# Performance work log

Measured on AMD Instinct MI355X. Metric: run time of the kernel, lower is better.

The kernel has to match this reference:

```python
import jax, jax.numpy as jnp
import numpy as np
import itertools

R = 32  # voxel resolution
B, CIN, COUT, N, SD = 4, 32, 64, 32768, 256


def group_norm(x, gamma, beta, eps=1e-5):
    # torch GroupNorm with g = min(8, C) adjusted for divisibility
    C = x.shape[1]
    g = min(8, C)
    while g > 1 and C % g:
        g -= 1
    b = x.shape[0]
    xs = x.reshape(b, g, C // g, -1)
    mu = xs.mean(axis=(2, 3), keepdims=True)
    var = xs.var(axis=(2, 3), keepdims=True)
    xn = ((xs - mu) / jnp.sqrt(var + eps)).reshape(x.shape)
    shp = (1, C) + (1,) * (x.ndim - 2)
    return xn * gamma.reshape(shp) + beta.reshape(shp)


def conv1x1(w, x):  # w: (O, C), x: (B, C, N)
    return jnp.einsum('oc,bcn->bon', w, x)


def conv3d(x, w):  # x: (B,C,D,H,W), w: (O,I,3,3,3), padding 1
    return jax.lax.conv_general_dilated(x, w, (1, 1, 1), 'SAME',
                                        dimension_numbers=('NCDHW', 'OIDHW', 'NCDHW'))


def normalize_coords(coords):  # (B,N,3) -> [0, R-1]
    vmin = coords.min(axis=1, keepdims=True)
    vmax = coords.max(axis=1, keepdims=True)
    return (coords - vmin) / jnp.maximum(vmax - vmin, 1e-8) * (R - 1)


def voxelize(feats_bcn, norm):  # average voxelization via scatter-add
    b, C, n = feats_bcn.shape
    idx = jnp.clip(jnp.round(norm), 0, R - 1).astype(jnp.int32)  # (B,N,3)
    flat = (idx[..., 0] * R + idx[..., 1]) * R + idx[..., 2]  # (B,N)
    f_bnc = feats_bcn.transpose(0, 2, 1)
    seg = jax.vmap(lambda f, i: jax.ops.segment_sum(f, i, num_segments=R ** 3))(f_bnc, flat)
    cnt = jax.vmap(lambda i: jax.ops.segment_sum(jnp.ones((n,), feats_bcn.dtype), i, num_segments=R ** 3))(flat)
    vox = seg / jnp.maximum(cnt, 1.0)[..., None]  # (B, R^3, C)
    return vox.transpose(0, 2, 1).reshape(b, C, R, R, R)


def devoxelize(vox, norm):  # trilinear interpolation gather
    b, C = vox.shape[:2]
    n = norm.shape[1]
    f = jnp.clip(norm, 0.0, R - 1)
    x0 = jnp.floor(f)
    fr = f - x0
    x0i = x0.astype(jnp.int32)
    idxs, wts = [], []
    for d in itertools.product((0, 1), repeat=3):
        dv = jnp.array(d, jnp.int32)
        ci = jnp.minimum(x0i + dv, R - 1)  # (B,N,3)
        w = jnp.prod(jnp.where(jnp.array(d, bool), fr, 1.0 - fr), axis=-1)  # (B,N)
        idxs.append((ci[..., 0] * R + ci[..., 1]) * R + ci[..., 2])
        wts.append(w)
    idx8 = jnp.stack(idxs, axis=-1)  # (B,N,8)
    w8 = jnp.stack(wts, axis=-1)  # (B,N,8)
    vf = vox.reshape(b, C, R ** 3)
    g = jnp.take_along_axis(vf, idx8.reshape(b, 1, n * 8), axis=2).reshape(b, C, n, 8)
    return jnp.einsum('bcnk,bnk->bcn', g, w8)


def setup_inputs() -> dict:
    key = jax.random.key(0)
    ks = jax.random.split(key, 12)
    s = 0.05
    return {
        'feats': jax.random.normal(ks[0], (B, CIN, N), jnp.float32),
        'coords': jax.random.uniform(ks[1], (B, N, 3), jnp.float32),
        'style': jax.random.normal(ks[2], (B, SD), jnp.float32),
        'w_pin': jax.random.normal(ks[3], (COUT, CIN), jnp.float32) * s,
        'g_pin': jnp.ones((COUT,), jnp.float32), 'b_pin': jnp.zeros((COUT,), jnp.float32),
        'w_v1': jax.random.normal(ks[4], (COUT, COUT, 3, 3, 3), jnp.float32) * s,
        'g_v1': jnp.ones((COUT,), jnp.float32), 'b_v1': jnp.zeros((COUT,), jnp.float32),
        'w_v2': jax.random.normal(ks[5], (COUT, COUT, 3, 3, 3), jnp.float32) * s,
        'g_v2': jnp.ones((COUT,), jnp.float32), 'b_v2': jnp.zeros((COUT,), jnp.float32),
        'w_fuse': jax.random.normal(ks[6], (COUT, COUT), jnp.float32) * s,
        'g_f': jnp.ones((COUT,), jnp.float32), 'b_f': jnp.zeros((COUT,), jnp.float32),
        'w_skip': jax.random.normal(ks[7], (COUT, CIN), jnp.float32) * s,
        'w_as': jax.random.normal(ks[8], (COUT, SD), jnp.float32) * s,
        'b_as': jnp.zeros((COUT,), jnp.float32),
        'w_ab': jax.random.normal(ks[9], (COUT, SD), jnp.float32) * s,
        'b_ab': jnp.zeros((COUT,), jnp.float32),
    }


def reference(feats, coords, style, w_pin, g_pin, b_pin, w_v1, g_v1, b_v1,
              w_v2, g_v2, b_v2, w_fuse, g_f, b_f, w_skip, w_as, b_as, w_ab, b_ab):
    silu = jax.nn.silu
    x_in = silu(group_norm(conv1x1(w_pin, feats), g_pin, b_pin))  # point_in
    norm = normalize_coords(coords)
    vox = voxelize(x_in, norm)
    vox = silu(group_norm(conv3d(vox, w_v1), g_v1, b_v1))
    vox = silu(group_norm(conv3d(vox, w_v2), g_v2, b_v2))
    devox = devoxelize(vox, norm)
    out = silu(group_norm(conv1x1(w_fuse, devox), g_f, b_f))  # fuse
    out = out + conv1x1(w_skip, feats)  # skip (c_in != c_out)
    s = (style @ w_as.T + b_as)[..., None]  # AdaIN scale (B, C, 1)
    bb = (style @ w_ab.T + b_ab)[..., None]
    return out * (1.0 + s) + bb
```

## Files before the change

kernel.cpp:

```cpp
#include <hip/hip_runtime.h>
#include <hip/hip_bf16.h>
#include <math.h>

#define RR   32
#define RB   4
#define CIN  32
#define CO   64
#define NP   32768
#define SD   256
#define NVOX (RR*RR*RR)
#define GRP  8
#define CPG  8
#define GN_CNT 262144.0f
#define PR   34
#define PSLICE (PR*PR*CO)
#define PROW   (PR*CO)
#define PVOL   ((size_t)PR*PR*PR*CO)

typedef __attribute__((ext_vector_type(8))) short short8;
typedef __attribute__((ext_vector_type(4))) float f32x4;
typedef __attribute__((ext_vector_type(16))) float f32x16;

__device__ inline float silu_f(float x){ return x / (1.f + __expf(-x)); }
__device__ inline float bf2f(ushort u){ uint v = ((uint)u)<<16; return *(float*)&v; }
__device__ inline ushort f2bf(float x){ __hip_bfloat16 h = __float2bfloat16(x); return *(ushort*)&h; }

__device__ inline void wpack_dev(const float* __restrict__ w, short* __restrict__ wp, int i){
    int l  = i & 63;
    int nt = (i>>6) & 1;
    int kc = (i>>7) & 3;
    int t  = i>>9;
    int oc = nt*32 + (l&31);
    int cib = kc*16 + (l>>5)*8;
    ushort out[8];
    #pragma unroll
    for (int j=0;j<8;j++) out[j] = f2bf(w[((oc*CO + cib + j))*27 + t]);
    *(uint4*)(wp + (size_t)i*8) = *(uint4*)out;
}

__global__ __launch_bounds__(256) void k_prep(const float* __restrict__ w_v1, const float* __restrict__ w_v2,
                      short* __restrict__ wp1, short* __restrict__ wp2,
                      const float* __restrict__ style, const float* __restrict__ w_as,
                      const float* __restrict__ b_as, const float* __restrict__ w_ab,
                      const float* __restrict__ b_ab, float* __restrict__ ada_s,
                      float* __restrict__ ada_b, float* __restrict__ stats,
                      const float* __restrict__ coords, float* __restrict__ vmm){
    __shared__ float smn[256][3], smx[256][3];
    int blk = blockIdx.x, t = threadIdx.x;
    if (blk < 54){
        int i = blk*256 + t;
        if (i < 27*4*2*64) wpack_dev(w_v1, wp1, i);
    } else if (blk < 108){
        int i = (blk-54)*256 + t;
        if (i < 27*4*2*64) wpack_dev(w_v2, wp2, i);
    } else if (blk == 108){
        stats[t] = 0.f;
        int b = t >> 6, o = t & 63;
        const float* st = style + b*SD;
        float accs = b_as[o], accb = b_ab[o];
        for (int k=0;k<SD;k++){ float sv = st[k]; accs += sv*w_as[o*SD+k]; accb += sv*w_ab[o*SD+k]; }
        ada_s[t]=accs; ada_b[t]=accb;
    } else {
        int b = blk - 109;
        float mn[3]={1e30f,1e30f,1e30f}, mx[3]={-1e30f,-1e30f,-1e30f};
        const float* cp = coords + (size_t)b*NP*3;
        for (int n=t;n<NP;n+=256){
            #pragma unroll
            for(int d=0;d<3;d++){ float v = cp[n*3+d]; mn[d]=fminf(mn[d],v); mx[d]=fmaxf(mx[d],v);}
        }
        #pragma unroll
        for(int d=0;d<3;d++){ smn[t][d]=mn[d]; smx[t][d]=mx[d]; }
        __syncthreads();
        for(int s=128;s>0;s>>=1){
            if(t<s){
                #pragma unroll
                for(int d=0;d<3;d++){
                    smn[t][d]=fminf(smn[t][d],smn[t+s][d]);
                    smx[t][d]=fmaxf(smx[t][d],smx[t+s][d]);
                }
            }
            __syncthreads();
        }
        if(t<3){ vmm[b*6+t]=smn[0][t]; vmm[b*6+3+t]=smx[0][t]; }
    }
}

__global__ __launch_bounds__(256) void k_count(const float* __restrict__ coords, const float* __restrict__ vmm,
                        int* __restrict__ pid, int* __restrict__ cnt){
    int p = blockIdx.x*256 + threadIdx.x;
    int b = p >> 15, n = p & (NP-1);
    const float* cp = coords + (size_t)(b*NP + n)*3;
    int id[3];
    #pragma unroll
    for(int d=0;d<3;d++){
        float vmin = vmm[b*6+d], vmax = vmm[b*6+3+d];
        float nr = (cp[d]-vmin)/fmaxf(vmax-vmin,1e-8f)*(RR-1);
        int ii = (int)rintf(nr);
        id[d] = min(max(ii,0),RR-1);
    }
    int flat = (id[0]*RR + id[1])*RR + id[2];
    pid[p] = flat;
    atomicAdd(&cnt[(b<<15)+flat], 1);
}

__global__ __launch_bounds__(1024) void k_scan(const int* __restrict__ cnt, int* __restrict__ offs,
                        int* __restrict__ cursor){
    int b = blockIdx.x, t = threadIdx.x;
    const int* c = cnt + (b<<15);
    int base = t*32;
    int pref[32];
    int s = 0;
    #pragma unroll
    for (int k4=0;k4<8;k4++){
        int4 q = *(const int4*)(c + base + k4*4);
        pref[k4*4+0]=s; s+=q.x;
        pref[k4*4+1]=s; s+=q.y;
        pref[k4*4+2]=s; s+=q.z;
        pref[k4*4+3]=s; s+=q.w;
    }
    int lane = t & 63, w = t >> 6;
    int inc = s;
    #pragma unroll
    for (int off=1; off<64; off<<=1){ int u = __shfl_up(inc, off); if (lane>=off) inc += u; }
    __shared__ int wsum[16];
    if (lane==63) wsum[w]=inc;
    __syncthreads();
    int wexcl=0;
    for (int i=0;i<w;i++) wexcl += wsum[i];
    int texcl = wexcl + inc - s;
    int* o = offs + (b<<15) + base;
    int* cu = cursor + (b<<15) + base;
    #pragma unroll
    for (int k=0;k<32;k++){ int v = texcl + pref[k]; o[k]=v; cu[k]=v; }
}

__global__ __launch_bounds__(256) void k_fill(const int* __restrict__ pid, int* __restrict__ cursor,
                       int* __restrict__ slotmap){
    int p = blockIdx.x*256 + threadIdx.x;
    int b = p >> 15;
    int v = pid[p];
    int slot = atomicAdd(&cursor[(b<<15)+v], 1);
    slotmap[p] = slot;
}

__global__ __launch_bounds__(256) void k_pin(const float* __restrict__ feats, const float* __restrict__ w_pin,
                      const int* __restrict__ slotmap,
                      ushort* __restrict__ ybuf, float* __restrict__ stats){
    __shared__ float sred[GRP*2];
    int t = threadIdx.x;
    if (t<GRP*2) sred[t]=0.f;
    __syncthreads();
    int l = t & 63, wv = t >> 6;
    int lc = l & 31, h = l >> 5;
    int p = blockIdx.x*128 + wv*32 + lc;
    int b = p >> 15, n = p & (NP-1);
    short8 aw[2][2];
    #pragma unroll
    for (int nt=0;nt<2;nt++)
    #pragma unroll
    for (int kc=0;kc<2;kc++){
        ushort tmp[8];
        #pragma unroll
        for (int j=0;j<8;j++) tmp[j]=f2bf(w_pin[(nt*32+lc)*CIN + kc*16 + h*8 + j]);
        aw[nt][kc]=*(short8*)tmp;
    }
    const float* fp = feats + (size_t)b*CIN*NP + n;
    short8 bf[2];
    #pragma unroll
    for (int kc=0;kc<2;kc++){
        ushort tmp[8];
        #pragma unroll
        for (int j=0;j<8;j++) tmp[j]=f2bf(fp[(size_t)(kc*16+h*8+j)*NP]);
        bf[kc]=*(short8*)tmp;
    }
    f32x16 acc0={}, acc1={};
    #pragma unroll
    for (int kc=0;kc<2;kc++){
        acc0 = __builtin_amdgcn_mfma_f32_32x32x16_bf16(aw[0][kc], bf[kc], acc0, 0,0,0);
        acc1 = __builtin_amdgcn_mfma_f32_32x32x16_bf16(aw[1][kc], bf[kc], acc1, 0,0,0);
    }
    int slot = slotmap[p];
    ushort* yo = ybuf + ((size_t)(b<<15) + slot)*CO;
    float sg[8], qg[8];
    #pragma unroll
    for (int nt=0;nt<2;nt++){
        #pragma unroll
        for (int q=0;q<4;q++){
            ushort pk[4]; float s=0.f, qq=0.f;
            #pragma unroll
            for (int j=0;j<4;j++){
                float v = nt ? acc1[q*4+j] : acc0[q*4+j];
                pk[j]=f2bf(v); s+=v; qq+=v*v;
            }
            *(uint2*)(yo + nt*32 + q*8 + h*4) = *(uint2*)pk;
            sg[nt*4+q]=s; qg[nt*4+q]=qq;
        }
    }
    #pragma unroll
    for (int g=0;g<8;g++){
        float s=sg[g], q=qg[g];
        #pragma unroll
        for (int off=1; off<64; off<<=1){ s+=__shfl_xor(s,off); q+=__shfl_xor(q,off); }
        if (l==0){ atomicAdd(&sred[g*2],s); atomicAdd(&sred[g*2+1],q); }
    }
    __syncthreads();
    if (t<GRP){ atomicAdd(&stats[(b*GRP+t)*2], sred[t*2]); atomicAdd(&stats[(b*GRP+t)*2+1], sred[t*2+1]); }
}

__global__ __launch_bounds__(256) void k_gather_pad(const ushort* __restrict__ ybuf, const int* __restrict__ offs,
                             const float* __restrict__ stats,
                             const float* __restrict__ gamma, const float* __restrict__ beta,
                             ushort* __restrict__ P){
    int i = blockIdx.x*256 + threadIdx.x;
    int c8 = i & 7;
    int vox = (i>>3) & (NVOX-1);
    int b = i >> 18;
    float s = stats[(b*GRP+c8)*2], qq = stats[(b*GRP+c8)*2+1];
    float m = s/GN_CNT;
    float inv = rsqrtf(qq/GN_CNT - m*m + 1e-5f);
    float ga[8], be[8];
    #pragma unroll
    for (int k=0;k<8;k++){ ga[k]=gamma[c8*8+k]*inv; be[k]=beta[c8*8+k]-m*ga[k]; }
    int o0 = offs[(b<<15)+vox];
    int o1 = (vox==NVOX-1) ? NP : offs[(b<<15)+vox+1];
    float acc[8];
    #pragma unroll
    for (int k=0;k<8;k++) acc[k]=0.f;
    for (int j=o0; j<o1; j++){
        uint4 raw = *(const uint4*)(ybuf + ((size_t)((b<<15)+j))*CO + c8*8);
        ushort* us = (ushort*)&raw;
        #pragma unroll
        for (int k=0;k<8;k++){
            float x = bf2f(us[k])*ga[k] + be[k];
            acc[k] += silu_f(x);
        }
    }
    float rc = (o1>o0) ? 1.f/(float)(o1-o0) : 0.f;
    ushort out[8];
    #pragma unroll
    for (int k=0;k<8;k++) out[k]=f2bf(acc[k]*rc);
    int u = vox>>10, v = (vox>>5)&31, w = vox&31;
    size_t pd = ((size_t)b*PVOL) + (size_t)(u+1)*PSLICE + (v+1)*PROW + (w+1)*CO + c8*8;
    *(uint4*)(P + pd) = *(uint4*)out;
}

__global__ __launch_bounds__(256, 2) void k_conv_mfma(const __hip_bfloat16* __restrict__ P,
                        const short* __restrict__ wpack,
                        __hip_bfloat16* __restrict__ outv, float* __restrict__ stats){
    __shared__ __align__(16) char lds[10*4352 + 24576];
    char* wlds = lds + 10*4352;
    int t = threadIdx.x;
    int blk = blockIdx.x;
    int vt = blk & 3;
    int u  = (blk >> 2) & 31;
    int b  = blk >> 7;
    int v0 = vt*8;

    const ushort* Pp = (const ushort*)P;
    int l  = t & 63;
    int wv = t >> 6;
    int lr = l & 31;
    int lh = l >> 5;

    f32x16 acc00 = {}, acc01 = {}, acc10 = {}, acc11 = {};

    for (int dz = 0; dz < 3; dz++){
        for (int i = t; i < 2720; i += 256){
            int r = i / 272;
            int chunk = i - r*272;
            size_t src = (size_t)b*PVOL + (size_t)(u+dz)*PSLICE + (size_t)(v0+r)*PROW + (size_t)chunk*8;
            uint4 val = *(const uint4*)(Pp + src);
            int vx = chunk >> 3;
            int colb = (chunk & 7) << 4;
            *(uint4*)(lds + r*4352 + vx*128 + (colb ^ ((vx&7)<<4))) = val;
        }
        for (int dy = 0; dy < 3; dy++){
            const uint4* wsrc = (const uint4*)(wpack + (size_t)(dz*9 + dy*3)*4096);
            uint4* wdst = (uint4*)wlds;
            #pragma unroll
            for (int i=0;i<6;i++) wdst[t + i*256] = wsrc[t + i*256];
            __syncthreads();
            #pragma unroll
            for (int dx = 0; dx < 3; dx++){
                int vx = lr + dx;
                int sw = (vx & 7) << 4;
                int ra = (2*wv + dy)*4352 + vx*128;
                int wb = dx*8192 + l*16;
                #pragma unroll
                for (int kc = 0; kc < 4; kc++){
                    short8 bw0 = *(const short8*)(wlds + wb + kc*2048);
                    short8 bw1 = *(const short8*)(wlds + wb + kc*2048 + 1024);
                    int col = (kc*32 + lh*16) ^ sw;
                    short8 av0 = *(const short8*)(lds + ra + col);
                    short8 av1 = *(const short8*)(lds + ra + 4352 + col);
                    acc00 = __builtin_amdgcn_mfma_f32_32x32x16_bf16(av0, bw0, acc00, 0, 0, 0);
                    acc01 = __builtin_amdgcn_mfma_f32_32x32x16_bf16(av0, bw1, acc01, 0, 0, 0);
                    acc10 = __builtin_amdgcn_mfma_f32_32x32x16_bf16(av1, bw0, acc10, 0, 0, 0);
                    acc11 = __builtin_amdgcn_mfma_f32_32x32x16_bf16(av1, bw1, acc11, 0, 0, 0);
                }
            }
            __syncthreads();
        }
    }

    ushort* ob = (ushort*)outv;
    float s0 = 0.f, q0 = 0.f, s1 = 0.f, q1 = 0.f;
    size_t vrow0 = ((size_t)(b*32 + u)*32 + v0 + 2*wv);
    #pragma unroll
    for (int reg = 0; reg < 16; reg++){
        int x = (reg&3) + 8*(reg>>2) + 4*lh;
        float a, c;
        a = acc00[reg]; c = acc01[reg];
        s0 += a; q0 += a*a; s1 += c; q1 += c*c;
        ob[(vrow0*32 + x)*CO + lr]      = f2bf(a);
        ob[(vrow0*32 + x)*CO + 32 + lr] = f2bf(c);
        a = acc10[reg]; c = acc11[reg];
        s0 += a; q0 += a*a; s1 += c; q1 += c*c;
        ob[((vrow0+1)*32 + x)*CO + lr]      = f2bf(a);
        ob[((vrow0+1)*32 + x)*CO + 32 + lr] = f2bf(c);
    }
    #pragma unroll
    for (int off : {1,2,4,32}){
        s0 += __shfl_xor(s0, off); q0 += __shfl_xor(q0, off);
        s1 += __shfl_xor(s1, off); q1 += __shfl_xor(q1, off);
    }
    if (lh==0 && (lr&7)==0){
        int g0 = lr>>3;
        atomicAdd(&stats[(b*GRP+g0)*2],     s0);
        atomicAdd(&stats[(b*GRP+g0)*2+1],   q0);
        atomicAdd(&stats[(b*GRP+4+g0)*2],   s1);
        atomicAdd(&stats[(b*GRP+4+g0)*2+1], q1);
    }
}

__global__ __launch_bounds__(256) void k_gnfin_cast(const __hip_bfloat16* __restrict__ raw, const float* __restrict__ stats,
                        const float* __restrict__ gamma, const float* __restrict__ beta,
                        __hip_bfloat16* __restrict__ P){
    int i = blockIdx.x*256 + threadIdx.x;
    int c8 = i & 7;
    int vox = (i>>3) & (NVOX-1);
    int b = i >> 18;
    float s = stats[(b*GRP+c8)*2], qq = stats[(b*GRP+c8)*2+1];
    float m = s/GN_CNT;
    float inv = rsqrtf(qq/GN_CNT - m*m + 1e-5f);
    uint4 rv = *(const uint4*)((const ushort*)raw + ((size_t)i)*8);
    ushort* us = (ushort*)&rv;
    ushort out[8];
    #pragma unroll
    for (int j=0;j<8;j++){
        int c = c8*8+j;
        float x = (bf2f(us[j]) - m)*inv*gamma[c] + beta[c];
        out[j] = f2bf(silu_f(x));
    }
    int u = vox>>10, v = (vox>>5)&31, w = vox&31;
    size_t pd = ((size_t)b*PVOL) + (size_t)(u+1)*PSLICE + (v+1)*PROW + (w+1)*CO + c8*8;
    *(uint4*)((ushort*)P + pd) = *(uint4*)out;
}

__global__ __launch_bounds__(256) void k_devox_fuse(const __hip_bfloat16* __restrict__ vox_, const float* __restrict__ coords,
                             const float* __restrict__ vmm, const float* __restrict__ wf,
                             const float* __restrict__ st2, const float* __restrict__ g_v2,
                             const float* __restrict__ b_v2,
                             ushort* __restrict__ obuf, float* __restrict__ stats){
    __shared__ float sred[GRP*2];
    int t = threadIdx.x;
    if (t<GRP*2) sred[t]=0.f;
    __syncthreads();
    int l = t & 63, wv = t >> 6;
    int lc = l & 31, h = l >> 5;
    int p = blockIdx.x*128 + wv*32 + lc;
    int b = p >> 15, n = p & (NP-1);
    short8 aw[2][4];
    #pragma unroll
    for (int nt=0;nt<2;nt++)
    #pragma unroll
    for (int kc=0;kc<4;kc++){
        ushort tmp[8];
        #pragma unroll
        for (int j=0;j<8;j++) tmp[j]=f2bf(wf[(nt*32+lc)*CO + kc*16 + h*8 + j]);
        aw[nt][kc]=*(short8*)tmp;
    }
    float ga[4][8], be[4][8];
    #pragma unroll
    for (int kc=0;kc<4;kc++){
        int g = kc*2 + h;
        float s = st2[(b*GRP+g)*2], qq = st2[(b*GRP+g)*2+1];
        float m = s/GN_CNT;
        float inv = rsqrtf(qq/GN_CNT - m*m + 1e-5f);
        #pragma unroll
        for (int j=0;j<8;j++){
            int c = kc*16 + h*8 + j;
            ga[kc][j] = g_v2[c]*inv;
            be[kc][j] = b_v2[c] - m*ga[kc][j];
        }
    }
    const float* cp = coords + (size_t)(b*NP+n)*3;
    float fr[3]; int x0[3];
    #pragma unroll
    for(int d=0;d<3;d++){
        float vmin=vmm[b*6+d], vmax=vmm[b*6+3+d];
        float nr = (cp[d]-vmin)/fmaxf(vmax-vmin,1e-8f)*(RR-1);
        nr = fminf(fmaxf(nr,0.f),(float)(RR-1));
        float fl = floorf(nr);
        x0[d]=(int)fl; fr[d]=nr-fl;
    }
    float dev[4][8] = {};
    const ushort* vb = (const ushort*)vox_ + (size_t)b*NVOX*CO;
    #pragma unroll
    for (int k=0;k<8;k++){
        int d0=(k>>2)&1, d1=(k>>1)&1, d2=k&1;
        int i0=min(x0[0]+d0,RR-1), i1=min(x0[1]+d1,RR-1), i2=min(x0[2]+d2,RR-1);
        float w = (d0?fr[0]:1.f-fr[0])*(d1?fr[1]:1.f-fr[1])*(d2?fr[2]:1.f-fr[2]);
        const ushort* vp = vb + (size_t)((i0*RR+i1)*RR+i2)*CO + h*8;
        #pragma unroll
        for (int kc=0;kc<4;kc++){
            uint4 rv = *(const uint4*)(vp + kc*16);
            ushort* us = (ushort*)&rv;
            #pragma unroll
            for (int j=0;j<8;j++){
                float x = bf2f(us[j])*ga[kc][j] + be[kc][j];
                dev[kc][j] += w * silu_f(x);
            }
        }
    }
    short8 bf[4];
    #pragma unroll
    for (int kc=0;kc<4;kc++){
        ushort tmp[8];
        #pragma unroll
        for (int j=0;j<8;j++) tmp[j]=f2bf(dev[kc][j]);
        bf[kc]=*(short8*)tmp;
    }
    f32x16 acc0={}, acc1={};
    #pragma unroll
    for (int kc=0;kc<4;kc++){
        acc0 = __builtin_amdgcn_mfma_f32_32x32x16_bf16(aw[0][kc], bf[kc], acc0, 0,0,0);
        acc1 = __builtin_amdgcn_mfma_f32_32x32x16_bf16(aw[1][kc], bf[kc], acc1, 0,0,0);
    }
    ushort* op = obuf + (size_t)p*CO;
    float sg[8], qg[8];
    #pragma unroll
    for (int nt=0;nt<2;nt++){
        #pragma unroll
        for (int q=0;q<4;q++){
            ushort pk[4]; float s=0.f, qq=0.f;
            #pragma unroll
            for (int j=0;j<4;j++){
                float v = nt ? acc1[q*4+j] : acc0[q*4+j];
                pk[j]=f2bf(v); s+=v; qq+=v*v;
            }
            *(uint2*)(op + nt*32 + q*8 + h*4) = *(uint2*)pk;
            sg[nt*4+q]=s; qg[nt*4+q]=qq;
        }
    }
    #pragma unroll
    for (int g=0;g<8;g++){
        float s=sg[g], q=qg[g];
        #pragma unroll
        for (int off=1; off<64; off<<=1){ s+=__shfl_xor(s,off); q+=__shfl_xor(q,off); }
        if (l==0){ atomicAdd(&sred[g*2],s); atomicAdd(&sred[g*2+1],q); }
    }
    __syncthreads();
    if (t<GRP){ atomicAdd(&stats[(b*GRP+t)*2], sred[t*2]); atomicAdd(&stats[(b*GRP+t)*2+1], sred[t*2+1]); }
}

__global__ __launch_bounds__(256) void k_final(const ushort* __restrict__ obuf, const float* __restrict__ stats,
                        const float* __restrict__ gamma, const float* __restrict__ beta,
                        const float* __restrict__ feats, const float* __restrict__ wskip,
                        const float* __restrict__ ada_s, const float* __restrict__ ada_b,
                        float* __restrict__ out){
    int t = threadIdx.x;
    int l = t & 63, wv = t >> 6;
    int lc = l & 31, h = l >> 5;
    int p = blockIdx.x*128 + wv*32 + lc;
    int b = p >> 15, n = p & (NP-1);
    short8 aw[2][2];
    #pragma unroll
    for (int nt=0;nt<2;nt++)
    #pragma unroll
    for (int kc=0;kc<2;kc++){
        ushort tmp[8];
        #pragma unroll
        for (int j=0;j<8;j++) tmp[j]=f2bf(wskip[(nt*32+lc)*CIN + kc*16 + h*8 + j]);
        aw[nt][kc]=*(short8*)tmp;
    }
    const float* fp = feats + (size_t)b*CIN*NP + n;
    short8 bf[2];
    #pragma unroll
    for (int kc=0;kc<2;kc++){
        ushort tmp[8];
        #pragma unroll
        for (int j=0;j<8;j++) tmp[j]=f2bf(fp[(size_t)(kc*16+h*8+j)*NP]);
        bf[kc]=*(short8*)tmp;
    }
    f32x16 acc0={}, acc1={};
    #pragma unroll
    for (int kc=0;kc<2;kc++){
        acc0 = __builtin_amdgcn_mfma_f32_32x32x16_bf16(aw[0][kc], bf[kc], acc0, 0,0,0);
        acc1 = __builtin_amdgcn_mfma_f32_32x32x16_bf16(aw[1][kc], bf[kc], acc1, 0,0,0);
    }
    float mean[GRP], inv[GRP];
    #pragma unroll
    for (int g=0; g<GRP; g++){
        float s=stats[(b*GRP+g)*2], q=stats[(b*GRP+g)*2+1];
        float m=s/GN_CNT;
        mean[g]=m; inv[g]=rsqrtf(q/GN_CNT - m*m + 1e-5f);
    }
    const ushort* ip = obuf + (size_t)p*CO;
    float* op = out + (size_t)b*CO*NP + n;
    #pragma unroll
    for (int nt=0;nt<2;nt++){
        #pragma unroll
        for (int q=0;q<4;q++){
            uint2 raw = *(const uint2*)(ip + nt*32 + q*8 + h*4);
            ushort* us = (ushort*)&raw;
            int g = nt*4 + q;
            #pragma unroll
            for (int j=0;j<4;j++){
                int oc = nt*32 + q*8 + h*4 + j;
                float u = (bf2f(us[j]) - mean[g])*inv[g]*gamma[oc] + beta[oc];
                u = silu_f(u);
                float sk = nt ? acc1[q*4+j] : acc0[q*4+j];
                float s = ada_s[b*CO+oc], bb = ada_b[b*CO+oc];
                op[(size_t)oc*NP] = (u+sk)*(1.f+s)+bb;
            }
        }
    }
}

extern "C" void kernel_launch(void* const* d_in, const int* in_sizes, int n_in,
                              void* d_out, int out_size, void* d_ws, size_t ws_size,
                              hipStream_t stream){
    const float* feats =(const float*)d_in[0];
    const float* coords=(const float*)d_in[1];
    const float* style =(const float*)d_in[2];
    const float* w_pin =(const float*)d_in[3];
    const float* g_pin =(const float*)d_in[4];
    const float* b_pin =(const float*)d_in[5];
    const float* w_v1  =(const float*)d_in[6];
    const float* g_v1  =(const float*)d_in[7];
    const float* b_v1  =(const float*)d_in[8];
    const float* w_v2  =(const float*)d_in[9];
    const float* g_v2  =(const float*)d_in[10];
    const float* b_v2  =(const float*)d_in[11];
    const float* w_fuse=(const float*)d_in[12];
    const float* g_f   =(const float*)d_in[13];
    const float* b_f   =(const float*)d_in[14];
    const float* w_skip=(const float*)d_in[15];
    const float* w_as  =(const float*)d_in[16];
    const float* b_as  =(const float*)d_in[17];
    const float* w_ab  =(const float*)d_in[18];
    const float* b_ab  =(const float*)d_in[19];
    float* out=(float*)d_out;
    char* ws =(char*)d_ws;

    ushort* ybuf  = (ushort*)ws;
    ushort* Pvol  = (ushort*)(ws + 16777216);
    ushort* raw   = (ushort*)(ws + 16777216 + 20123648);
    char*   small = ws + 16777216 + 20123648 + 16777216;
    float* stats  = (float*)small;
    float* vmm    = stats + 256;
    float* ada_s  = vmm + 24;
    float* ada_b  = ada_s + RB*CO;
    short* wp1    = (short*)(ada_b + RB*CO);
    short* wp2    = wp1 + 27*4*2*64*8;
    int*   pid    = (int*)(wp2 + 27*4*2*64*8);
    int*   cnt    = pid + RB*NP;
    int*   offs   = cnt + RB*NVOX;
    int*   cursor = offs + RB*NVOX;
    int*   slotmap= cursor + RB*NVOX;
    ushort* obuf  = ybuf;

    float* st0 = stats;
    float* st1 = stats + 64;
    float* st2 = stats + 128;
    float* st3 = stats + 192;

    hipMemsetAsync(cnt, 0, (size_t)RB*NVOX*sizeof(int), stream);
    hipMemsetAsync(Pvol, 0, (size_t)RB*PVOL*sizeof(ushort), stream);

    k_prep<<<113,256,0,stream>>>(w_v1,w_v2,wp1,wp2,style,w_as,b_as,w_ab,b_ab,
                                 ada_s,ada_b,stats,coords,vmm);
    k_count<<<RB*NP/256,256,0,stream>>>(coords,vmm,pid,cnt);
    k_scan<<<RB,1024,0,stream>>>(cnt,offs,cursor);
    k_fill<<<RB*NP/256,256,0,stream>>>(pid,cursor,slotmap);
    k_pin<<<RB*NP/128,256,0,stream>>>(feats,w_pin,slotmap,ybuf,st0);
    k_gather_pad<<<RB*NVOX*8/256,256,0,stream>>>(ybuf,offs,st0,g_pin,b_pin,Pvol);

    k_conv_mfma<<<RB*RR*4,256,0,stream>>>((const __hip_bfloat16*)Pvol, wp1, (__hip_bfloat16*)raw, st1);
    k_gnfin_cast<<<RB*NVOX*8/256,256,0,stream>>>((const __hip_bfloat16*)raw, st1, g_v1, b_v1, (__hip_bfloat16*)Pvol);
    k_conv_mfma<<<RB*RR*4,256,0,stream>>>((const __hip_bfloat16*)Pvol, wp2, (__hip_bfloat16*)raw, st2);

    k_devox_fuse<<<RB*NP/128,256,0,stream>>>((const __hip_bfloat16*)raw, coords, vmm, w_fuse,
                                             st2, g_v2, b_v2, obuf, st3);
    k_final<<<RB*NP/128,256,0,stream>>>(obuf, st3, g_f, b_f, feats, w_skip, ada_s, ada_b, out);
}
```

Before: 385.5 us.

## Process devoxelization in voxel-sorted point order for gather locality

Normalized coordinates are computed once in k_count and scattered into voxel-sorted order in k_fill. k_devox_fuse then walks points in sorted order, so neighbouring threads read nearby voxels in the trilinear gather. k_final maps each point back through slotmap to read the fused output. This adds an extra scattered float4 write pass and an indirect read in the final kernel, and the workspace must be large enough for the two new float4 buffers.

```diff
diff --git a/kernel.cpp b/kernel.cpp
--- a/kernel.cpp
+++ b/kernel.cpp
@@ -86,20 +86,23 @@
 }
 
 __global__ __launch_bounds__(256) void k_count(const float* __restrict__ coords, const float* __restrict__ vmm,
-                        int* __restrict__ pid, int* __restrict__ cnt){
+                        int* __restrict__ pid, int* __restrict__ cnt, float4* __restrict__ nrm){
     int p = blockIdx.x*256 + threadIdx.x;
     int b = p >> 15, n = p & (NP-1);
     const float* cp = coords + (size_t)(b*NP + n)*3;
     int id[3];
+    float nc[3];
     #pragma unroll
     for(int d=0;d<3;d++){
         float vmin = vmm[b*6+d], vmax = vmm[b*6+3+d];
         float nr = (cp[d]-vmin)/fmaxf(vmax-vmin,1e-8f)*(RR-1);
+        nc[d] = fminf(fmaxf(nr,0.f),(float)(RR-1));
         int ii = (int)rintf(nr);
         id[d] = min(max(ii,0),RR-1);
     }
     int flat = (id[0]*RR + id[1])*RR + id[2];
     pid[p] = flat;
+    nrm[p] = make_float4(nc[0],nc[1],nc[2],0.f);
     atomicAdd(&cnt[(b<<15)+flat], 1);
 }
 
@@ -135,12 +138,14 @@
 }
 
 __global__ __launch_bounds__(256) void k_fill(const int* __restrict__ pid, int* __restrict__ cursor,
-                       int* __restrict__ slotmap){
+                       int* __restrict__ slotmap, const float4* __restrict__ nrm,
+                       float4* __restrict__ nrm_s){
     int p = blockIdx.x*256 + threadIdx.x;
     int b = p >> 15;
     int v = pid[p];
     int slot = atomicAdd(&cursor[(b<<15)+v], 1);
     slotmap[p] = slot;
+    nrm_s[(b<<15)+slot] = nrm[p];
 }
 
 __global__ __launch_bounds__(256) void k_pin(const float* __restrict__ feats, const float* __restrict__ w_pin,
@@ -357,8 +362,8 @@
     *(uint4*)((ushort*)P + pd) = *(uint4*)out;
 }
 
-__global__ __launch_bounds__(256) void k_devox_fuse(const __hip_bfloat16* __restrict__ vox_, const float* __restrict__ coords,
-                             const float* __restrict__ vmm, const float* __restrict__ wf,
+__global__ __launch_bounds__(256) void k_devox_fuse(const __hip_bfloat16* __restrict__ vox_,
+                             const float4* __restrict__ nrm_s, const float* __restrict__ wf,
                              const float* __restrict__ st2, const float* __restrict__ g_v2,
                              const float* __restrict__ b_v2,
                              ushort* __restrict__ obuf, float* __restrict__ stats){
@@ -368,8 +373,8 @@
     __syncthreads();
     int l = t & 63, wv = t >> 6;
     int lc = l & 31, h = l >> 5;
-    int p = blockIdx.x*128 + wv*32 + lc;
-    int b = p >> 15, n = p & (NP-1);
+    int j_ = blockIdx.x*128 + wv*32 + lc;
+    int b = j_ >> 15;
     short8 aw[2][4];
     #pragma unroll
     for (int nt=0;nt<2;nt++)
@@ -394,15 +399,13 @@
             be[kc][j] = b_v2[c] - m*ga[kc][j];
         }
     }
-    const float* cp = coords + (size_t)(b*NP+n)*3;
+    float4 nr4 = nrm_s[j_];
+    float f3[3] = {nr4.x, nr4.y, nr4.z};
     float fr[3]; int x0[3];
     #pragma unroll
     for(int d=0;d<3;d++){
-        float vmin=vmm[b*6+d], vmax=vmm[b*6+3+d];
-        float nr = (cp[d]-vmin)/fmaxf(vmax-vmin,1e-8f)*(RR-1);
-        nr = fminf(fmaxf(nr,0.f),(float)(RR-1));
-        float fl = floorf(nr);
-        x0[d]=(int)fl; fr[d]=nr-fl;
+        float fl = floorf(f3[d]);
+        x0[d]=(int)fl; fr[d]=f3[d]-fl;
     }
     float dev[4][8] = {};
     const ushort* vb = (const ushort*)vox_ + (size_t)b*NVOX*CO;
@@ -437,7 +440,7 @@
         acc0 = __builtin_amdgcn_mfma_f32_32x32x16_bf16(aw[0][kc], bf[kc], acc0, 0,0,0);
         acc1 = __builtin_amdgcn_mfma_f32_32x32x16_bf16(aw[1][kc], bf[kc], acc1, 0,0,0);
     }
-    ushort* op = obuf + (size_t)p*CO;
+    ushort* op = obuf + (size_t)j_*CO;
     float sg[8], qg[8];
     #pragma unroll
     for (int nt=0;nt<2;nt++){
@@ -464,7 +467,8 @@
     if (t<GRP){ atomicAdd(&stats[(b*GRP+t)*2], sred[t*2]); atomicAdd(&stats[(b*GRP+t)*2+1], sred[t*2+1]); }
 }
 
-__global__ __launch_bounds__(256) void k_final(const ushort* __restrict__ obuf, const float* __restrict__ stats,
+__global__ __launch_bounds__(256) void k_final(const ushort* __restrict__ obuf, const int* __restrict__ slotmap,
+                        const float* __restrict__ stats,
                         const float* __restrict__ gamma, const float* __restrict__ beta,
                         const float* __restrict__ feats, const float* __restrict__ wskip,
                         const float* __restrict__ ada_s, const float* __restrict__ ada_b,
@@ -506,7 +510,8 @@
         float m=s/GN_CNT;
         mean[g]=m; inv[g]=rsqrtf(q/GN_CNT - m*m + 1e-5f);
     }
-    const ushort* ip = obuf + (size_t)p*CO;
+    int slot = slotmap[p];
+    const ushort* ip = obuf + ((size_t)(b<<15) + slot)*CO;
     float* op = out + (size_t)b*CO*NP + n;
     #pragma unroll
     for (int nt=0;nt<2;nt++){
@@ -569,6 +574,8 @@
     int*   offs   = cnt + RB*NVOX;
     int*   cursor = offs + RB*NVOX;
     int*   slotmap= cursor + RB*NVOX;
+    float4* nrm4  = (float4*)(slotmap + RB*NP);
+    float4* nrm_s = nrm4 + RB*NP;
     ushort* obuf  = ybuf;
 
     float* st0 = stats;
@@ -581,9 +588,9 @@
 
     k_prep<<<113,256,0,stream>>>(w_v1,w_v2,wp1,wp2,style,w_as,b_as,w_ab,b_ab,
                                  ada_s,ada_b,stats,coords,vmm);
-    k_count<<<RB*NP/256,256,0,stream>>>(coords,vmm,pid,cnt);
+    k_count<<<RB*NP/256,256,0,stream>>>(coords,vmm,pid,cnt,nrm4);
     k_scan<<<RB,1024,0,stream>>>(cnt,offs,cursor);
-    k_fill<<<RB*NP/256,256,0,stream>>>(pid,cursor,slotmap);
+    k_fill<<<RB*NP/256,256,0,stream>>>(pid,cursor,slotmap,nrm4,nrm_s);
     k_pin<<<RB*NP/128,256,0,stream>>>(feats,w_pin,slotmap,ybuf,st0);
     k_gather_pad<<<RB*NVOX*8/256,256,0,stream>>>(ybuf,offs,st0,g_pin,b_pin,Pvol);
 
@@ -591,7 +598,7 @@
     k_gnfin_cast<<<RB*NVOX*8/256,256,0,stream>>>((const __hip_bfloat16*)raw, st1, g_v1, b_v1, (__hip_bfloat16*)Pvol);
     k_conv_mfma<<<RB*RR*4,256,0,stream>>>((const __hip_bfloat16*)Pvol, wp2, (__hip_bfloat16*)raw, st2);
 
-    k_devox_fuse<<<RB*NP/128,256,0,stream>>>((const __hip_bfloat16*)raw, coords, vmm, w_fuse,
+    k_devox_fuse<<<RB*NP/128,256,0,stream>>>((const __hip_bfloat16*)raw, nrm_s, w_fuse,
                                              st2, g_v2, b_v2, obuf, st3);
-    k_final<<<RB*NP/128,256,0,stream>>>(obuf, st3, g_f, b_f, feats, w_skip, ada_s, ada_b, out);
-}
+    k_final<<<RB*NP/128,256,0,stream>>>(obuf, slotmap, st3, g_f, b_f, feats, w_skip, ada_s, ada_b, out);
+}
```

Result: no change. 385.7 us (+0.1%).
